# Kernel tuning notes

Hardware: AMD Instinct MI355X
Metric: run time of the kernel (lower is better)

## Reference

```python
import jax, jax.numpy as jnp
import numpy as np

B, E, CIN, O = 2, 50000, 8, 128


def _mesh_conv(x, gemm, w, b):
    # MeshCNN MeshConv: x (B,C,E), gemm (B,E,4) neighbor indices, w (O,C,5), b (O,)
    # gather 4 GeMM neighbors per edge, build 5 symmetric features, 1x5 conv
    neigh = jax.vmap(lambda xb, gb: xb[:, gb])(x, gemm)  # (B,C,E,4)
    f1, f2, f3, f4 = neigh[..., 0], neigh[..., 1], neigh[..., 2], neigh[..., 3]
    G = jnp.stack([x, f1 + f3, f2 + f4, jnp.abs(f1 - f3), jnp.abs(f2 - f4)], axis=-1)  # (B,C,E,5)
    return jnp.einsum('bces,ocs->boe', G, w) + b[None, :, None]


def _inorm(x, eps=1e-5):
    # InstanceNorm (no affine, biased variance) over the edge dim, per (batch, channel)
    m = jnp.mean(x, axis=-1, keepdims=True)
    v = jnp.var(x, axis=-1, keepdims=True)
    return (x - m) * jax.lax.rsqrt(v + eps)


def _conv1(x, w, b):
    # 1x1 Conv1d: x (B,C,E), w (O,C)
    return jnp.einsum('bce,oc->boe', x, w) + b[None, :, None]


def setup_inputs() -> dict:
    key = jax.random.key(0)
    ks = jax.random.split(key, 16)

    def W(k, shape, fan):
        return jax.random.normal(k, shape, jnp.float32) * np.float32(1.0 / np.sqrt(fan))

    d = {}
    d['fe'] = jax.random.normal(ks[0], (B, CIN, E), jnp.float32)
    d['gemm'] = jax.random.randint(ks[1], (B, E, 4), 0, E)
    # first-stage MeshConvs: geometry branch (5 ch) and position branch (3 ch)
    d['w_e1'] = W(ks[2], (O, 5, 5), 25);       d['b_e1'] = jnp.zeros((O,), jnp.float32)
    d['w_p1'] = W(ks[3], (O, 3, 5), 15);       d['b_p1'] = jnp.zeros((O,), jnp.float32)
    # residual-block MeshConvs (blocks=1)
    d['w_e2'] = W(ks[4], (O, O, 5), O * 5);    d['b_e2'] = jnp.zeros((O,), jnp.float32)
    d['w_p2'] = W(ks[5], (O, O, 5), O * 5);    d['b_p2'] = jnp.zeros((O,), jnp.float32)
    # Attn(in_dim=O)
    d['wa'] = W(ks[6], (O // 4, O), O);        d['ba'] = jnp.zeros((O // 4,), jnp.float32)
    d['wb'] = W(ks[7], (O // 4, O), O);        d['bb'] = jnp.zeros((O // 4,), jnp.float32)
    d['wal'] = W(ks[8], (O // 2, O // 2), O // 2);  d['bal'] = jnp.zeros((O // 2,), jnp.float32)
    d['wbl'] = W(ks[9], (O // 2, O // 2), O // 2);  d['bbl'] = jnp.zeros((O // 2,), jnp.float32)
    d['wat'] = W(ks[10], (O // 2, O // 2, 5), O // 2 * 5); d['bat'] = jnp.zeros((O // 2,), jnp.float32)
    d['wbt'] = W(ks[11], (O // 2, O // 2, 5), O // 2 * 5); d['bbt'] = jnp.zeros((O // 2,), jnp.float32)
    d['waf'] = W(ks[12], (O, O), O);           d['baf'] = jnp.zeros((O,), jnp.float32)
    d['wbf'] = W(ks[13], (O, O), O);           d['bbf'] = jnp.zeros((O,), jnp.float32)
    return d


def reference(fe, gemm, w_e1, b_e1, w_p1, b_p1, w_e2, b_e2, w_p2, b_p2,
              wa, ba, wb, bb, wal, bal, wbl, bbl, wat, bat, wbt, bbt,
              waf, baf, wbf, bbf):
    # DownConv (8-channel input path): split into edge (5) and point (3) branches
    fe_e, fe_p = fe[:, :5, :], fe[:, 5:, :]
    x1_e = jax.nn.relu(_inorm(_mesh_conv(fe_e, gemm, w_e1, b_e1)))
    x2_e = jax.nn.relu(_inorm(_mesh_conv(x1_e, gemm, w_e2, b_e2)) + x1_e)
    x1_p = jax.nn.relu(_inorm(_mesh_conv(fe_p, gemm, w_p1, b_p1)))
    x2_p = jax.nn.relu(_inorm(_mesh_conv(x1_p, gemm, w_p2, b_p2)) + x1_p)
    # Attn fusion
    x_all = jnp.concatenate([_conv1(x2_e, wa, ba), _conv1(x2_p, wb, bb)], axis=1)  # (B, O/2, E)
    x_a_two = jnp.concatenate([_conv1(x_all, wal, bal), _mesh_conv(x_all, gemm, wat, bat)], axis=1)
    x_b_two = jnp.concatenate([_conv1(x_all, wbl, bbl), _mesh_conv(x_all, gemm, wbt, bbt)], axis=1)
    wA = jax.nn.sigmoid(_inorm(_conv1(x_a_two, waf, baf)))  # (B,O,E)
    wB = jax.nn.sigmoid(_inorm(_conv1(x_b_two, wbf, bbf)))
    weights = jax.nn.softmax(jnp.stack([wA, wB], axis=1), axis=1)  # (B,2,O,E)
    agg = x2_e * weights[:, 0] + x2_p * weights[:, 1]
    # x2_ep = cat(x2_e, x2_p); also emit the attention-fused combine (before_pool)
    return jnp.concatenate([x2_e, x2_p, agg], axis=1)  # (B, 3*O, E)
```

## Files before the change

### kernel.cpp

```cpp
#include <hip/hip_runtime.h>
#include <cstdio>
#include <math.h>


#define E_TOT 50000
#define B_TOT 2
#define TILE_E 64
#define NBLK ((E_TOT + TILE_E - 1) / TILE_E)

typedef _Float16 half_t;
typedef __attribute__((ext_vector_type(4))) _Float16 h4;
typedef __attribute__((ext_vector_type(8))) _Float16 h8;
typedef __attribute__((ext_vector_type(4))) float f32x4;

__device__ __forceinline__ float sigmoidf_(float x) {
    return 1.0f / (1.0f + __expf(-x));
}
__device__ __forceinline__ h8 habs8(h8 x) {
    union { h8 h; unsigned int u[4]; } v;
    v.h = x;
#pragma unroll
    for (int i = 0; i < 4; ++i) v.u[i] &= 0x7FFF7FFFu;
    return v.h;
}

#define OFF_W1E   0
#define OFF_W1P   8192
#define OFF_WTE2  16384
#define OFF_WTP2  98304
#define OFF_WHA   180224
#define OFF_WHB   221184
#define OFF_WTA   262144
#define OFF_WTB   266240
#define OFF_WTAF  270336
#define OFF_WTBF  286720
#define WARENA_N  303104

__global__ __launch_bounds__(256)
void wprep_k(half_t* __restrict__ wa_,
             const float* __restrict__ w_e1, const float* __restrict__ w_p1,
             const float* __restrict__ w_e2, const float* __restrict__ w_p2,
             const float* __restrict__ wat,  const float* __restrict__ wbt,
             const float* __restrict__ wa,   const float* __restrict__ wb,
             const float* __restrict__ wal,  const float* __restrict__ wbl,
             const float* __restrict__ waf,  const float* __restrict__ wbf)
{
    int idx = blockIdx.x * 256 + threadIdx.x;
    switch (blockIdx.y) {
    case 0: if (idx < 8192) { int o = idx >> 6, k = idx & 63, s = k >> 3, cc = k & 7;
            float v = (s < 5 && cc < 5) ? w_e1[o * 25 + cc * 5 + s] : 0.f;
            wa_[OFF_W1E + idx] = (half_t)v; } break;
    case 1: if (idx < 8192) { int o = idx >> 6, k = idx & 63, s = k >> 3, cc = k & 7;
            float v = (s < 5 && cc >= 5) ? w_p1[o * 15 + (cc - 5) * 5 + s] : 0.f;
            wa_[OFF_W1P + idx] = (half_t)v; } break;
    case 2: if (idx < 81920) { int o = idx / 640, r = idx % 640, s = r >> 7, c = r & 127;
            wa_[OFF_WTE2 + idx] = (half_t)w_e2[(o * 128 + c) * 5 + s]; } break;
    case 3: if (idx < 81920) { int o = idx / 640, r = idx % 640, s = r >> 7, c = r & 127;
            wa_[OFF_WTP2 + idx] = (half_t)w_p2[(o * 128 + c) * 5 + s]; } break;
    case 4: if (idx < 40960) { int o = idx / 320, r = idx % 320, s = r >> 6, c = r & 63;
            float v = (o < 64) ? (s == 0 ? wal[o * 64 + c] : 0.f)
                               : wat[((o - 64) * 64 + c) * 5 + s];
            wa_[OFF_WHA + idx] = (half_t)v; } break;
    case 5: if (idx < 40960) { int o = idx / 320, r = idx % 320, s = r >> 6, c = r & 63;
            float v = (o < 64) ? (s == 0 ? wbl[o * 64 + c] : 0.f)
                               : wbt[((o - 64) * 64 + c) * 5 + s];
            wa_[OFF_WHB + idx] = (half_t)v; } break;
    case 6: if (idx < 4096)  wa_[OFF_WTA  + idx] = (half_t)wa[idx];  break;
    case 7: if (idx < 4096)  wa_[OFF_WTB  + idx] = (half_t)wb[idx];  break;
    case 8: if (idx < 16384) wa_[OFF_WTAF + idx] = (half_t)waf[idx]; break;
    case 9: if (idx < 16384) wa_[OFF_WTBF + idx] = (half_t)wbf[idx]; break;
    }
}

__global__ __launch_bounds__(256)
void transpose_in_k(const float* __restrict__ fe, float* __restrict__ fet)
{
    int b = blockIdx.z;
    int e = blockIdx.x * 256 + threadIdx.x;
    if (e >= E_TOT) return;
    float v[8];
#pragma unroll
    for (int c = 0; c < 8; ++c)
        v[c] = fe[((long)b * 8 + c) * E_TOT + e];
    float4* dst = (float4*)&fet[((long)b * E_TOT + e) * 8];
    dst[0] = make_float4(v[0], v[1], v[2], v[3]);
    dst[1] = make_float4(v[4], v[5], v[6], v[7]);
}

__global__ __launch_bounds__(512)
void mesh1_both_k(const float* __restrict__ fet, const int* __restrict__ gemm,
                  const half_t* __restrict__ war,
                  const float* __restrict__ be1, const float* __restrict__ bp1,
                  half_t* __restrict__ tmpe, half_t* __restrict__ tmpp,
                  float* __restrict__ parte, float* __restrict__ partp)
{
    __shared__ h8 Gl[64 * 8];
    __shared__ int nidx[64][4];

    const int tid  = threadIdx.x;
    const int b    = blockIdx.y;
    const int e0   = blockIdx.x * TILE_E;
    const int lane = tid & 63;
    const int wv   = tid >> 6;
    const int l15  = lane & 15;
    const int kg   = lane >> 4;
    const int br   = wv >> 2;
    const int o0   = (wv & 3) * 32;

    const float* xb = fet + (long)b * E_TOT * 8;

    if (tid < 256) {
        int e = tid >> 2, s = tid & 3;
        int eg = e0 + e;
        nidx[e][s] = (eg < E_TOT) ? gemm[((long)b * E_TOT + eg) * 4 + s] : 0;
    }
    __syncthreads();

    {
        int e = tid >> 3, g = tid & 7;
        int eg = e0 + e;
        int se = (eg < E_TOT) ? eg : 0;
        h8 r;
        if (g == 0) {
            const float* p = xb + (long)se * 8;
            float4 v0 = *(const float4*)p, v1 = *(const float4*)(p + 4);
            r[0] = (half_t)v0.x; r[1] = (half_t)v0.y; r[2] = (half_t)v0.z; r[3] = (half_t)v0.w;
            r[4] = (half_t)v1.x; r[5] = (half_t)v1.y; r[6] = (half_t)v1.z; r[7] = (half_t)v1.w;
        } else if (g <= 4) {
            int ia = (g == 1 || g == 3) ? 0 : 1;
            const float* pa = xb + (long)nidx[e][ia] * 8;
            const float* pb = xb + (long)nidx[e][ia + 2] * 8;
            float4 a0 = *(const float4*)pa, a1 = *(const float4*)(pa + 4);
            float4 b0 = *(const float4*)pb, b1 = *(const float4*)(pb + 4);
            float aa[8] = {a0.x, a0.y, a0.z, a0.w, a1.x, a1.y, a1.z, a1.w};
            float bb[8] = {b0.x, b0.y, b0.z, b0.w, b1.x, b1.y, b1.z, b1.w};
            if (g <= 2) {
#pragma unroll
                for (int j = 0; j < 8; ++j) r[j] = (half_t)(aa[j] + bb[j]);
            } else {
#pragma unroll
                for (int j = 0; j < 8; ++j) r[j] = (half_t)fabsf(aa[j] - bb[j]);
            }
        } else {
#pragma unroll
            for (int j = 0; j < 8; ++j) r[j] = (half_t)0.f;
        }
        Gl[(e * 8 + g) ^ (e & 7)] = r;
    }
    __syncthreads();

    f32x4 acc[4][2];
#pragma unroll
    for (int mt = 0; mt < 4; ++mt)
#pragma unroll
        for (int nt = 0; nt < 2; ++nt)
#pragma unroll
            for (int j = 0; j < 4; ++j) acc[mt][nt][j] = 0.f;

    const half_t* wt = war + (br ? OFF_W1P : OFF_W1E);
#pragma unroll
    for (int ks = 0; ks < 2; ++ks) {
        h8 bw[2];
#pragma unroll
        for (int nt = 0; nt < 2; ++nt)
            bw[nt] = *(const h8*)(wt + (long)(o0 + nt * 16 + l15) * 64 + ks * 32 + kg * 8);
#pragma unroll
        for (int mt = 0; mt < 4; ++mt) {
            int row = mt * 16 + l15;
            h8 a = Gl[row * 8 + ((ks * 4 + kg) ^ (row & 7))];
#pragma unroll
            for (int nt = 0; nt < 2; ++nt)
                acc[mt][nt] = __builtin_amdgcn_mfma_f32_16x16x32_f16(a, bw[nt], acc[mt][nt], 0, 0, 0);
        }
    }

    const float* bias = br ? bp1 : be1;
    half_t* yb = (br ? tmpp : tmpe) + (long)b * E_TOT * 128;
    float* part = br ? partp : parte;
    float bv[2], s1[2], s2[2];
#pragma unroll
    for (int nt = 0; nt < 2; ++nt) {
        bv[nt] = bias[o0 + nt * 16 + l15];
        s1[nt] = 0.f; s2[nt] = 0.f;
    }
#pragma unroll
    for (int mt = 0; mt < 4; ++mt) {
        int ebase = e0 + mt * 16 + (kg << 2);
#pragma unroll
        for (int j = 0; j < 4; ++j) {
            if (ebase + j < E_TOT) {
#pragma unroll
                for (int nt = 0; nt < 2; ++nt) {
                    float v = acc[mt][nt][j] + bv[nt];
                    yb[(long)(ebase + j) * 128 + o0 + nt * 16 + l15] = (half_t)v;
                    s1[nt] += v; s2[nt] += v * v;
                }
            }
        }
    }
#pragma unroll
    for (int nt = 0; nt < 2; ++nt) {
        s1[nt] += __shfl_xor(s1[nt], 16); s1[nt] += __shfl_xor(s1[nt], 32);
        s2[nt] += __shfl_xor(s2[nt], 16); s2[nt] += __shfl_xor(s2[nt], 32);
    }
    if (lane < 16) {
        long pb = ((long)b * NBLK + blockIdx.x) * 128;
#pragma unroll
        for (int nt = 0; nt < 2; ++nt) {
            part[(pb + o0 + nt * 16 + lane) * 2 + 0] = s1[nt];
            part[(pb + o0 + nt * 16 + lane) * 2 + 1] = s2[nt];
        }
    }
}

__global__ __launch_bounds__(512)
void mesh2_both_k(const half_t* __restrict__ x1e, const half_t* __restrict__ x1p,
                  const int* __restrict__ gemm, const half_t* __restrict__ war,
                  const float* __restrict__ be, const float* __restrict__ bp,
                  half_t* __restrict__ tmpe, half_t* __restrict__ tmpp,
                  float* __restrict__ parte, float* __restrict__ partp)
{
    __shared__ h8 GlA[64 * 16];
    __shared__ h8 GlB[64 * 16];
    __shared__ int nidx[64][4];

    const int tid  = threadIdx.x;
    const int br   = blockIdx.y;
    const int b    = blockIdx.z;
    const int e0   = blockIdx.x * TILE_E;
    const int lane = tid & 63;
    const int wv   = tid >> 6;
    const int l15  = lane & 15;
    const int kg   = lane >> 4;
    const int o0   = wv * 16;

    const half_t* xb = (br ? x1p : x1e) + (long)b * E_TOT * 128;
    const half_t* wt = war + (br ? OFF_WTP2 : OFF_WTE2);

    if (tid < 256) {
        int e = tid >> 2, s = tid & 3;
        int eg = e0 + e;
        nidx[e][s] = (eg < E_TOT) ? gemm[((long)b * E_TOT + eg) * 4 + s] : 0;
    }

    auto stage_self = [&](h8* dst) {
#pragma unroll
        for (int t = 0; t < 2; ++t) {
            int q = t * 512 + tid;
            int e = q >> 4, c8 = q & 15;
            int eg = e0 + e;
            int se = (eg < E_TOT) ? eg : 0;
            dst[(e * 16 + c8) ^ (e & 7)] = *(const h8*)(xb + (long)se * 128 + c8 * 8);
        }
    };
    auto stage_pair = [&](h8* dstS, h8* dstD, int ia, int ib) {
#pragma unroll
        for (int t = 0; t < 2; ++t) {
            int q = t * 512 + tid;
            int e = q >> 4, c8 = q & 15;
            int na = nidx[e][ia], nb = nidx[e][ib];
            h8 a  = *(const h8*)(xb + (long)na * 128 + c8 * 8);
            h8 bq = *(const h8*)(xb + (long)nb * 128 + c8 * 8);
            int slot = (e * 16 + c8) ^ (e & 7);
            dstS[slot] = a + bq;
            dstD[slot] = habs8(a - bq);
        }
    };

    f32x4 acc[4];
#pragma unroll
    for (int mt = 0; mt < 4; ++mt)
#pragma unroll
        for (int j = 0; j < 4; ++j) acc[mt][j] = 0.f;

    auto compute_chunk = [&](const h8* buf, int s) {
#pragma unroll
        for (int ks = 0; ks < 4; ++ks) {
            h8 bw = *(const h8*)(wt + ((long)(o0 + l15) * 5 + s) * 128 + ks * 32 + kg * 8);
#pragma unroll
            for (int mt = 0; mt < 4; ++mt) {
                int row = mt * 16 + l15;
                h8 a = buf[row * 16 + ((ks * 4 + kg) ^ (row & 7))];
                acc[mt] = __builtin_amdgcn_mfma_f32_16x16x32_f16(a, bw, acc[mt], 0, 0, 0);
            }
        }
    };

    stage_self(GlA);
    __syncthreads();
    compute_chunk(GlA, 0);
    __syncthreads();
    stage_pair(GlA, GlB, 0, 2);
    __syncthreads();
    compute_chunk(GlA, 1);
    compute_chunk(GlB, 3);
    __syncthreads();
    stage_pair(GlA, GlB, 1, 3);
    __syncthreads();
    compute_chunk(GlA, 2);
    compute_chunk(GlB, 4);

    const float* bias = br ? bp : be;
    half_t* yb = (br ? tmpp : tmpe) + (long)b * E_TOT * 128;
    float* part = br ? partp : parte;
    float bv = bias[o0 + l15];
    float s1 = 0.f, s2 = 0.f;
#pragma unroll
    for (int mt = 0; mt < 4; ++mt) {
        int ebase = e0 + mt * 16 + (kg << 2);
#pragma unroll
        for (int j = 0; j < 4; ++j) {
            if (ebase + j < E_TOT) {
                float v = acc[mt][j] + bv;
                yb[(long)(ebase + j) * 128 + o0 + l15] = (half_t)v;
                s1 += v; s2 += v * v;
            }
        }
    }
    s1 += __shfl_xor(s1, 16); s1 += __shfl_xor(s1, 32);
    s2 += __shfl_xor(s2, 16); s2 += __shfl_xor(s2, 32);
    if (lane < 16) {
        long pb = ((long)b * NBLK + blockIdx.x) * 128;
        part[(pb + o0 + lane) * 2 + 0] = s1;
        part[(pb + o0 + lane) * 2 + 1] = s2;
    }
}

__global__ __launch_bounds__(512)
void heads_k(const half_t* __restrict__ xall, const int* __restrict__ gemm,
             const half_t* __restrict__ war,
             const float* __restrict__ bal, const float* __restrict__ bbl,
             const float* __restrict__ bat, const float* __restrict__ bbt,
             half_t* __restrict__ xa2, half_t* __restrict__ xb2)
{
    __shared__ h8 GlA[64 * 8];
    __shared__ h8 GlB[64 * 8];
    __shared__ int nidx[64][4];

    const int tid  = threadIdx.x;
    const int br   = blockIdx.y;
    const int b    = blockIdx.z;
    const int e0   = blockIdx.x * TILE_E;
    const int lane = tid & 63;
    const int wv   = tid >> 6;
    const int l15  = lane & 15;
    const int kg   = lane >> 4;
    const int o0   = wv * 16;

    const half_t* xb = xall + (long)b * E_TOT * 64;
    const half_t* wt = war + (br ? OFF_WHB : OFF_WHA);

    if (tid < 256) {
        int e = tid >> 2, s = tid & 3;
        int eg = e0 + e;
        nidx[e][s] = (eg < E_TOT) ? gemm[((long)b * E_TOT + eg) * 4 + s] : 0;
    }

    auto stage_self = [&](h8* dst) {
        int q = tid;
        int e = q >> 3, c8 = q & 7;
        int eg = e0 + e;
        int se = (eg < E_TOT) ? eg : 0;
        dst[(e * 8 + c8) ^ (e & 7)] = *(const h8*)(xb + (long)se * 64 + c8 * 8);
    };
    auto stage_pair = [&](h8* dstS, h8* dstD, int ia, int ib) {
        int q = tid;
        int e = q >> 3, c8 = q & 7;
        int na = nidx[e][ia], nb = nidx[e][ib];
        h8 a  = *(const h8*)(xb + (long)na * 64 + c8 * 8);
        h8 bq = *(const h8*)(xb + (long)nb * 64 + c8 * 8);
        int slot = (e * 8 + c8) ^ (e & 7);
        dstS[slot] = a + bq;
        dstD[slot] = habs8(a - bq);
    };

    f32x4 acc[4];
#pragma unroll
    for (int mt = 0; mt < 4; ++mt)
#pragma unroll
        for (int j = 0; j < 4; ++j) acc[mt][j] = 0.f;

    auto compute_chunk = [&](const h8* buf, int s) {
#pragma unroll
        for (int ks = 0; ks < 2; ++ks) {
            h8 bw = *(const h8*)(wt + ((long)(o0 + l15) * 5 + s) * 64 + ks * 32 + kg * 8);
#pragma unroll
            for (int mt = 0; mt < 4; ++mt) {
                int row = mt * 16 + l15;
                h8 a = buf[row * 8 + ((ks * 4 + kg) ^ (row & 7))];
                acc[mt] = __builtin_amdgcn_mfma_f32_16x16x32_f16(a, bw, acc[mt], 0, 0, 0);
            }
        }
    };

    stage_self(GlA);
    __syncthreads();
    compute_chunk(GlA, 0);
    __syncthreads();
    stage_pair(GlA, GlB, 0, 2);
    __syncthreads();
    compute_chunk(GlA, 1);
    compute_chunk(GlB, 3);
    __syncthreads();
    stage_pair(GlA, GlB, 1, 3);
    __syncthreads();
    compute_chunk(GlA, 2);
    compute_chunk(GlB, 4);

    int o = o0 + l15;
    float bv = (o < 64) ? (br ? bbl[o] : bal[o]) : (br ? bbt[o - 64] : bat[o - 64]);
    half_t* yb = (br ? xb2 : xa2) + (long)b * E_TOT * 128;
#pragma unroll
    for (int mt = 0; mt < 4; ++mt) {
        int ebase = e0 + mt * 16 + (kg << 2);
#pragma unroll
        for (int j = 0; j < 4; ++j) {
            if (ebase + j < E_TOT)
                yb[(long)(ebase + j) * 128 + o] = (half_t)(acc[mt][j] + bv);
        }
    }
}

__global__ __launch_bounds__(512)
void gates_k(const half_t* __restrict__ xa2, const half_t* __restrict__ xb2,
             const half_t* __restrict__ war,
             const float* __restrict__ baf, const float* __restrict__ bbf,
             half_t* __restrict__ tmpe, half_t* __restrict__ tmpp,
             float* __restrict__ parte, float* __restrict__ partp)
{
    __shared__ h8 Gl[64 * 16];

    const int tid  = threadIdx.x;
    const int br   = blockIdx.y;
    const int b    = blockIdx.z;
    const int e0   = blockIdx.x * TILE_E;
    const int lane = tid & 63;
    const int wv   = tid >> 6;
    const int l15  = lane & 15;
    const int kg   = lane >> 4;
    const int o0   = wv * 16;

    const half_t* xb = (br ? xb2 : xa2) + (long)b * E_TOT * 128;
    const half_t* wt = war + (br ? OFF_WTBF : OFF_WTAF);

#pragma unroll
    for (int t = 0; t < 2; ++t) {
        int q = t * 512 + tid;
        int e = q >> 4, c8 = q & 15;
        int eg = e0 + e;
        int se = (eg < E_TOT) ? eg : 0;
        Gl[(e * 16 + c8) ^ (e & 7)] = *(const h8*)(xb + (long)se * 128 + c8 * 8);
    }
    __syncthreads();

    f32x4 acc[4];
#pragma unroll
    for (int mt = 0; mt < 4; ++mt)
#pragma unroll
        for (int j = 0; j < 4; ++j) acc[mt][j] = 0.f;

#pragma unroll
    for (int ks = 0; ks < 4; ++ks) {
        h8 bw = *(const h8*)(wt + (long)(o0 + l15) * 128 + ks * 32 + kg * 8);
#pragma unroll
        for (int mt = 0; mt < 4; ++mt) {
            int row = mt * 16 + l15;
            h8 a = Gl[row * 16 + ((ks * 4 + kg) ^ (row & 7))];
            acc[mt] = __builtin_amdgcn_mfma_f32_16x16x32_f16(a, bw, acc[mt], 0, 0, 0);
        }
    }

    const float* bias = br ? bbf : baf;
    half_t* yb = (br ? tmpp : tmpe) + (long)b * E_TOT * 128;
    float* part = br ? partp : parte;
    float bv = bias[o0 + l15];
    float s1 = 0.f, s2 = 0.f;
#pragma unroll
    for (int mt = 0; mt < 4; ++mt) {
        int ebase = e0 + mt * 16 + (kg << 2);
#pragma unroll
        for (int j = 0; j < 4; ++j) {
            if (ebase + j < E_TOT) {
                float v = acc[mt][j] + bv;
                yb[(long)(ebase + j) * 128 + o0 + l15] = (half_t)v;
                s1 += v; s2 += v * v;
            }
        }
    }
    s1 += __shfl_xor(s1, 16); s1 += __shfl_xor(s1, 32);
    s2 += __shfl_xor(s2, 16); s2 += __shfl_xor(s2, 32);
    if (lane < 16) {
        long pb = ((long)b * NBLK + blockIdx.x) * 128;
        part[(pb + o0 + lane) * 2 + 0] = s1;
        part[(pb + o0 + lane) * 2 + 1] = s2;
    }
}

__global__ __launch_bounds__(256)
void xall_k(const half_t* __restrict__ x2e, const half_t* __restrict__ x2p,
            const half_t* __restrict__ war,
            const float* __restrict__ ba, const float* __restrict__ bb,
            half_t* __restrict__ xall)
{
    __shared__ h8 Gl[64 * 16];

    const int tid  = threadIdx.x;
    const int br   = blockIdx.y;
    const int b    = blockIdx.z;
    const int e0   = blockIdx.x * TILE_E;
    const int lane = tid & 63;
    const int wv   = tid >> 6;
    const int l15  = lane & 15;
    const int kg   = lane >> 4;
    const int eoff = wv * 16;

    const half_t* xb = (br ? x2p : x2e) + (long)b * E_TOT * 128;
    const half_t* wt = war + (br ? OFF_WTB : OFF_WTA);

#pragma unroll
    for (int t = 0; t < 4; ++t) {
        int q = t * 256 + tid;
        int e = q >> 4, c8 = q & 15;
        int eg = e0 + e;
        int se = (eg < E_TOT) ? eg : 0;
        Gl[(e * 16 + c8) ^ (e & 7)] = *(const h8*)(xb + (long)se * 128 + c8 * 8);
    }
    __syncthreads();

    f32x4 acc[2];
#pragma unroll
    for (int nt = 0; nt < 2; ++nt)
#pragma unroll
        for (int j = 0; j < 4; ++j) acc[nt][j] = 0.f;

#pragma unroll
    for (int ks = 0; ks < 4; ++ks) {
        h8 bw[2];
#pragma unroll
        for (int nt = 0; nt < 2; ++nt)
            bw[nt] = *(const h8*)(wt + (long)(nt * 16 + l15) * 128 + ks * 32 + kg * 8);
        int row = eoff + l15;
        h8 a = Gl[row * 16 + ((ks * 4 + kg) ^ (row & 7))];
#pragma unroll
        for (int nt = 0; nt < 2; ++nt)
            acc[nt] = __builtin_amdgcn_mfma_f32_16x16x32_f16(a, bw[nt], acc[nt], 0, 0, 0);
    }

    const float* bias = br ? bb : ba;
    half_t* yb = xall + (long)b * E_TOT * 64;
    int oOff = br * 32;
#pragma unroll
    for (int nt = 0; nt < 2; ++nt) {
        float bv = bias[nt * 16 + l15];
        int ebase = e0 + eoff + (kg << 2);
#pragma unroll
        for (int j = 0; j < 4; ++j) {
            if (ebase + j < E_TOT)
                yb[(long)(ebase + j) * 64 + oOff + nt * 16 + l15] = (half_t)(acc[nt][j] + bv);
        }
    }
}

__global__ __launch_bounds__(256)
void stats2_k(const float* __restrict__ parte, const float* __restrict__ partp,
              float* __restrict__ statse, float* __restrict__ statsp)
{
    int g = blockIdx.x;
    int br = g >> 8, rem = g & 255, b = rem >> 7, o = rem & 127;
    const float* part = br ? partp : parte;
    float* stats = br ? statsp : statse;
    int tid = threadIdx.x;
    float s1 = 0.f, s2 = 0.f;
    for (int k = tid; k < NBLK; k += 256) {
        long base = (((long)b * NBLK + k) * 128 + o) * 2;
        s1 += part[base];
        s2 += part[base + 1];
    }
#pragma unroll
    for (int d = 1; d < 64; d <<= 1) {
        s1 += __shfl_xor(s1, d);
        s2 += __shfl_xor(s2, d);
    }
    __shared__ float r1[4], r2[4];
    int wv = tid >> 6;
    if ((tid & 63) == 0) { r1[wv] = s1; r2[wv] = s2; }
    __syncthreads();
    if (tid == 0) {
        s1 = r1[0] + r1[1] + r1[2] + r1[3];
        s2 = r2[0] + r2[1] + r2[2] + r2[3];
        float mean = s1 / (float)E_TOT;
        float var  = s2 / (float)E_TOT - mean * mean;
        var = fmaxf(var, 0.f);
        stats[(b * 128 + o) * 2 + 0] = mean;
        stats[(b * 128 + o) * 2 + 1] = rsqrtf(var + 1e-5f);
    }
}

__global__ __launch_bounds__(256)
void norm_act2_k(const half_t* __restrict__ tmpe, const half_t* __restrict__ tmpp,
                 const float* __restrict__ statse, const float* __restrict__ statsp,
                 half_t* __restrict__ x1e, half_t* __restrict__ x1p)
{
    const long PER = (long)B_TOT * E_TOT * 16;
    long q = (long)blockIdx.x * 256 + threadIdx.x;
    if (q >= 2 * PER) return;
    int br = (q >= PER);
    q -= (long)br * PER;
    const half_t* src = br ? tmpp : tmpe;
    const float* stats = br ? statsp : statse;
    half_t* dst = br ? x1p : x1e;
    long idx = q * 8;
    int c = (int)(idx & 127);
    int b = (int)((idx >> 7) / E_TOT);
    h8 v = *(const h8*)&src[idx];
    h8 r;
#pragma unroll
    for (int j = 0; j < 8; ++j) {
        float2 st = *(const float2*)&stats[(b * 128 + c + j) * 2];
        float t = ((float)v[j] - st.x) * st.y;
        r[j] = (half_t)fmaxf(t, 0.f);
    }
    *(h8*)&dst[idx] = r;
}

__global__ __launch_bounds__(256)
void normres2_k(const half_t* __restrict__ tmpe, const half_t* __restrict__ tmpp,
                const half_t* __restrict__ x1e, const half_t* __restrict__ x1p,
                const float* __restrict__ statse, const float* __restrict__ statsp,
                float* __restrict__ outb,
                half_t* __restrict__ x2e, half_t* __restrict__ x2p)
{
    __shared__ float T[32 * 68];
    int br = blockIdx.y >> 2, cg = blockIdx.y & 3;
    int b = blockIdx.z;
    int e0 = blockIdx.x * 64;
    int tid = threadIdx.x;
    const half_t* xin = br ? tmpp : tmpe;
    const half_t* res = br ? x1p : x1e;
    const float* stats = br ? statsp : statse;
    half_t* x2b = br ? x2p : x2e;
    int sect = br * 128;
#pragma unroll
    for (int i = 0; i < 2; ++i) {
        int q = tid + i * 256;
        int e = q >> 3, cq = q & 7;
        int eg = e0 + e;
        int se = (eg < E_TOT) ? eg : (E_TOT - 1);
        int c = cg * 32 + cq * 4;
        long base = ((long)b * E_TOT + se) * 128 + c;
        h4 v4 = *(const h4*)&xin[base];
        h4 r4 = *(const h4*)&res[base];
        h4 o4;
#pragma unroll
        for (int j = 0; j < 4; ++j) {
            float2 st = *(const float2*)&stats[(b * 128 + c + j) * 2];
            float t = ((float)v4[j] - st.x) * st.y + (float)r4[j];
            t = fmaxf(t, 0.f);
            T[(cq * 4 + j) * 68 + e] = t;
            o4[j] = (half_t)t;
        }
        if (eg < E_TOT) *(h4*)&x2b[base] = o4;
    }
    __syncthreads();
#pragma unroll
    for (int i = 0; i < 2; ++i) {
        int q = tid + i * 256;
        int cl = q >> 4, eq = q & 15;
        int e4 = e0 + eq * 4;
        int cglob = sect + cg * 32 + cl;
        float4 v = *(const float4*)&T[cl * 68 + eq * 4];
        long obase = ((long)b * 384 + cglob) * E_TOT + e4;
        if (e4 + 3 < E_TOT) {
            *(float4*)&outb[obase] = v;
        } else {
            const float* vp = &v.x;
            for (int j = 0; j < 4; ++j)
                if (e4 + j < E_TOT) outb[obase + j] = vp[j];
        }
    }
}

__global__ __launch_bounds__(256)
void gate_agg2_k(const half_t* __restrict__ tA, const half_t* __restrict__ tB,
                 const float* __restrict__ statsA, const float* __restrict__ statsB,
                 const half_t* __restrict__ x2e, const half_t* __restrict__ x2p,
                 float* __restrict__ outb)
{
    __shared__ float T[32 * 68];
    int b = blockIdx.z, cg = blockIdx.y;
    int e0 = blockIdx.x * 64;
    int tid = threadIdx.x;
#pragma unroll
    for (int i = 0; i < 2; ++i) {
        int q = tid + i * 256;
        int e = q >> 3, cq = q & 7;
        int eg = e0 + e;
        int se = (eg < E_TOT) ? eg : (E_TOT - 1);
        int c = cg * 32 + cq * 4;
        long base = ((long)b * E_TOT + se) * 128 + c;
        h4 a4 = *(const h4*)&tA[base];
        h4 b4 = *(const h4*)&tB[base];
        h4 xe4 = *(const h4*)&x2e[base];
        h4 xp4 = *(const h4*)&x2p[base];
#pragma unroll
        for (int j = 0; j < 4; ++j) {
            float2 sa = *(const float2*)&statsA[(b * 128 + c + j) * 2];
            float2 sb = *(const float2*)&statsB[(b * 128 + c + j) * 2];
            float na = sigmoidf_(((float)a4[j] - sa.x) * sa.y);
            float nb = sigmoidf_(((float)b4[j] - sb.x) * sb.y);
            float s = sigmoidf_(na - nb);
            T[(cq * 4 + j) * 68 + e] = (float)xe4[j] * s + (float)xp4[j] * (1.f - s);
        }
    }
    __syncthreads();
#pragma unroll
    for (int i = 0; i < 2; ++i) {
        int q = tid + i * 256;
        int cl = q >> 4, eq = q & 15;
        int e4 = e0 + eq * 4;
        int cglob = cg * 32 + cl;
        float4 v = *(const float4*)&T[cl * 68 + eq * 4];
        long ab = ((long)b * 384 + 256 + cglob) * E_TOT + e4;
        if (e4 + 3 < E_TOT) {
            *(float4*)&outb[ab] = v;
        } else {
            const float* vp = &v.x;
            for (int j = 0; j < 4; ++j)
                if (e4 + j < E_TOT) outb[ab + j] = vp[j];
        }
    }
}

extern "C" void kernel_launch(void* const* d_in, const int* in_sizes, int n_in,
                              void* d_out, int out_size, void* d_ws, size_t ws_size,
                              hipStream_t stream)
{
    const float* fe   = (const float*)d_in[0];
    const int*   gemm = (const int*)  d_in[1];
    const float* w_e1 = (const float*)d_in[2];  const float* b_e1 = (const float*)d_in[3];
    const float* w_p1 = (const float*)d_in[4];  const float* b_p1 = (const float*)d_in[5];
    const float* w_e2 = (const float*)d_in[6];  const float* b_e2 = (const float*)d_in[7];
    const float* w_p2 = (const float*)d_in[8];  const float* b_p2 = (const float*)d_in[9];
    const float* wa   = (const float*)d_in[10]; const float* ba   = (const float*)d_in[11];
    const float* wb   = (const float*)d_in[12]; const float* bb   = (const float*)d_in[13];
    const float* wal  = (const float*)d_in[14]; const float* bal  = (const float*)d_in[15];
    const float* wbl  = (const float*)d_in[16]; const float* bbl  = (const float*)d_in[17];
    const float* wat  = (const float*)d_in[18]; const float* bat  = (const float*)d_in[19];
    const float* wbt  = (const float*)d_in[20]; const float* bbt  = (const float*)d_in[21];
    const float* waf  = (const float*)d_in[22]; const float* baf  = (const float*)d_in[23];
    const float* wbf  = (const float*)d_in[24]; const float* bbf  = (const float*)d_in[25];
    float* out = (float*)d_out;

    const long EB = (long)E_TOT;

    char* wp = (char*)d_ws;
    auto alloc = [&](size_t bytes) -> void* {
        void* r = (void*)wp;
        wp += (bytes + 255) & ~(size_t)255;
        return r;
    };
    float*  FET    = (float*)alloc((size_t)B_TOT * EB * 8 * 4);
    half_t* TMP_E  = (half_t*)alloc((size_t)B_TOT * EB * 128 * 2);
    half_t* TMP_P  = (half_t*)alloc((size_t)B_TOT * EB * 128 * 2);
    half_t* X1E    = (half_t*)alloc((size_t)B_TOT * EB * 128 * 2);
    half_t* X1P    = (half_t*)alloc((size_t)B_TOT * EB * 128 * 2);
    half_t* X2E    = (half_t*)alloc((size_t)B_TOT * EB * 128 * 2);
    half_t* X2P    = (half_t*)alloc((size_t)B_TOT * EB * 128 * 2);
    half_t* XALL   = (half_t*)alloc((size_t)B_TOT * EB * 64 * 2);
    float*  PART_E = (float*)alloc((size_t)B_TOT * NBLK * 128 * 2 * 4);
    float*  PART_P = (float*)alloc((size_t)B_TOT * NBLK * 128 * 2 * 4);
    float*  STATSE = (float*)alloc((size_t)B_TOT * 128 * 2 * 4);
    float*  STATSP = (float*)alloc((size_t)B_TOT * 128 * 2 * 4);
    half_t* WAR    = (half_t*)alloc((size_t)WARENA_N * 2);

    if ((size_t)(wp - (char*)d_ws) > ws_size) {
        fprintf(stderr, "kernel_launch: ws too small (%zu < %zu)\n",
                ws_size, (size_t)(wp - (char*)d_ws));
        return;
    }

    half_t* XA2 = X1E;
    half_t* XB2 = X1P;

    dim3 blk256(256), blk512(512);
    dim3 gE2(NBLK, 2, B_TOT);
    dim3 gE1(NBLK, B_TOT);
    dim3 gT((E_TOT + 255) / 256, 1, B_TOT);
    dim3 gN8(NBLK, 8, B_TOT);
    dim3 gN4(NBLK, 4, B_TOT);
    int gA2 = (int)((2 * (long)B_TOT * EB * 16 + 255) / 256);

    wprep_k<<<dim3(320, 10, 1), blk256, 0, stream>>>(WAR,
        w_e1, w_p1, w_e2, w_p2, wat, wbt, wa, wb, wal, wbl, waf, wbf);
    transpose_in_k<<<gT, blk256, 0, stream>>>(fe, FET);

    mesh1_both_k<<<gE1, blk512, 0, stream>>>(FET, gemm, WAR, b_e1, b_p1,
        TMP_E, TMP_P, PART_E, PART_P);
    stats2_k<<<512, blk256, 0, stream>>>(PART_E, PART_P, STATSE, STATSP);
    norm_act2_k<<<gA2, blk256, 0, stream>>>(TMP_E, TMP_P, STATSE, STATSP, X1E, X1P);

    mesh2_both_k<<<gE2, blk512, 0, stream>>>(X1E, X1P, gemm, WAR, b_e2, b_p2,
        TMP_E, TMP_P, PART_E, PART_P);
    stats2_k<<<512, blk256, 0, stream>>>(PART_E, PART_P, STATSE, STATSP);
    normres2_k<<<gN8, blk256, 0, stream>>>(TMP_E, TMP_P, X1E, X1P, STATSE, STATSP,
        out, X2E, X2P);

    xall_k<<<gE2, blk256, 0, stream>>>(X2E, X2P, WAR, ba, bb, XALL);

    heads_k<<<gE2, blk512, 0, stream>>>(XALL, gemm, WAR, bal, bbl, bat, bbt, XA2, XB2);

    gates_k<<<gE2, blk512, 0, stream>>>(XA2, XB2, WAR, baf, bbf,
        TMP_E, TMP_P, PART_E, PART_P);
    stats2_k<<<512, blk256, 0, stream>>>(PART_E, PART_P, STATSE, STATSP);
    gate_agg2_k<<<gN4, blk256, 0, stream>>>(TMP_E, TMP_P, STATSE, STATSP,
        X2E, X2P, out);
}
```

Baseline: 363.1 us.

## Interleave x1 branches per edge and merge both branches into one gather block

Stores the two first-stage activations interleaved per edge (256 channels per row), so one block gathers neighbor rows for both edge and point branches in a single 512-byte access. Both branches are computed in one block with each wave covering 32 outputs, and the next neighbor pair is prefetched into registers during the MFMA compute of the current chunk. The heads kernel is restructured the same way so one block shares the gathered xall tile across both heads instead of gathering it twice. This cuts redundant random gathers and index loads, at the cost of more registers and LDS per block, a launch-bounds occupancy hint, and a strided write in the normalize kernel.

```diff
diff --git a/kernel.cpp b/kernel.cpp
--- a/kernel.cpp
+++ b/kernel.cpp
@@ -213,210 +213,259 @@
     }
 }
 
-__global__ __launch_bounds__(512)
-void mesh2_both_k(const half_t* __restrict__ x1e, const half_t* __restrict__ x1p,
-                  const int* __restrict__ gemm, const half_t* __restrict__ war,
-                  const float* __restrict__ be, const float* __restrict__ bp,
-                  half_t* __restrict__ tmpe, half_t* __restrict__ tmpp,
-                  float* __restrict__ parte, float* __restrict__ partp)
-{
-    __shared__ h8 GlA[64 * 16];
-    __shared__ h8 GlB[64 * 16];
+__global__ __launch_bounds__(512, 4)
+void mesh2i_k(const half_t* __restrict__ x1i, const int* __restrict__ gemm,
+              const half_t* __restrict__ war,
+              const float* __restrict__ be, const float* __restrict__ bp,
+              half_t* __restrict__ tmpe, half_t* __restrict__ tmpp,
+              float* __restrict__ parte, float* __restrict__ partp)
+{
+    __shared__ h8 B0[1024], B1[1024], B2[1024], B3[1024];
     __shared__ int nidx[64][4];
 
     const int tid  = threadIdx.x;
-    const int br   = blockIdx.y;
-    const int b    = blockIdx.z;
+    const int b    = blockIdx.y;
     const int e0   = blockIdx.x * TILE_E;
     const int lane = tid & 63;
     const int wv   = tid >> 6;
+    const int br   = wv >> 2;
+    const int o0   = (wv & 3) * 32;
     const int l15  = lane & 15;
     const int kg   = lane >> 4;
-    const int o0   = wv * 16;
-
-    const half_t* xb = (br ? x1p : x1e) + (long)b * E_TOT * 128;
-    const half_t* wt = war + (br ? OFF_WTP2 : OFF_WTE2);
+
+    const half_t* xb = x1i + (long)b * E_TOT * 256;
 
     if (tid < 256) {
         int e = tid >> 2, s = tid & 3;
         int eg = e0 + e;
         nidx[e][s] = (eg < E_TOT) ? gemm[((long)b * E_TOT + eg) * 4 + s] : 0;
     }
-
-    auto stage_self = [&](h8* dst) {
-#pragma unroll
-        for (int t = 0; t < 2; ++t) {
-            int q = t * 512 + tid;
-            int e = q >> 4, c8 = q & 15;
-            int eg = e0 + e;
-            int se = (eg < E_TOT) ? eg : 0;
-            dst[(e * 16 + c8) ^ (e & 7)] = *(const h8*)(xb + (long)se * 128 + c8 * 8);
-        }
-    };
-    auto stage_pair = [&](h8* dstS, h8* dstD, int ia, int ib) {
-#pragma unroll
-        for (int t = 0; t < 2; ++t) {
-            int q = t * 512 + tid;
-            int e = q >> 4, c8 = q & 15;
-            int na = nidx[e][ia], nb = nidx[e][ib];
-            h8 a  = *(const h8*)(xb + (long)na * 128 + c8 * 8);
-            h8 bq = *(const h8*)(xb + (long)nb * 128 + c8 * 8);
-            int slot = (e * 16 + c8) ^ (e & 7);
-            dstS[slot] = a + bq;
-            dstD[slot] = habs8(a - bq);
-        }
-    };
-
-    f32x4 acc[4];
+    __syncthreads();
+
+    int te[4], tc[4], tslot[4];
+#pragma unroll
+    for (int t = 0; t < 4; ++t) {
+        int q = t * 512 + tid;
+        te[t] = q >> 5; tc[t] = q & 31;
+        tslot[t] = (te[t] * 16 + (tc[t] & 15)) ^ (te[t] & 7);
+    }
+
+#pragma unroll
+    for (int t = 0; t < 4; ++t) {
+        int eg = e0 + te[t];
+        int se = (eg < E_TOT) ? eg : 0;
+        h8 v = *(const h8*)(xb + (long)se * 256 + tc[t] * 8);
+        ((tc[t] >> 4) ? B1 : B0)[tslot[t]] = v;
+    }
+    h8 rA[4], rB[4];
+#pragma unroll
+    for (int t = 0; t < 4; ++t) {
+        int na = nidx[te[t]][0], nb = nidx[te[t]][2];
+        rA[t] = *(const h8*)(xb + (long)na * 256 + tc[t] * 8);
+        rB[t] = *(const h8*)(xb + (long)nb * 256 + tc[t] * 8);
+    }
+    __syncthreads();
+
+    f32x4 acc[4][2];
 #pragma unroll
     for (int mt = 0; mt < 4; ++mt)
 #pragma unroll
-        for (int j = 0; j < 4; ++j) acc[mt][j] = 0.f;
-
-    auto compute_chunk = [&](const h8* buf, int s) {
+        for (int nt = 0; nt < 2; ++nt)
+#pragma unroll
+            for (int j = 0; j < 4; ++j) acc[mt][nt][j] = 0.f;
+
+    const half_t* wt = war + (br ? OFF_WTP2 : OFF_WTE2);
+    auto chunk = [&](const h8* bufE, const h8* bufP, int s) {
+        const h8* buf = br ? bufP : bufE;
 #pragma unroll
         for (int ks = 0; ks < 4; ++ks) {
-            h8 bw = *(const h8*)(wt + ((long)(o0 + l15) * 5 + s) * 128 + ks * 32 + kg * 8);
+            h8 bw0 = *(const h8*)(wt + ((long)(o0 + l15) * 5 + s) * 128 + ks * 32 + kg * 8);
+            h8 bw1 = *(const h8*)(wt + ((long)(o0 + 16 + l15) * 5 + s) * 128 + ks * 32 + kg * 8);
 #pragma unroll
             for (int mt = 0; mt < 4; ++mt) {
                 int row = mt * 16 + l15;
                 h8 a = buf[row * 16 + ((ks * 4 + kg) ^ (row & 7))];
-                acc[mt] = __builtin_amdgcn_mfma_f32_16x16x32_f16(a, bw, acc[mt], 0, 0, 0);
+                acc[mt][0] = __builtin_amdgcn_mfma_f32_16x16x32_f16(a, bw0, acc[mt][0], 0, 0, 0);
+                acc[mt][1] = __builtin_amdgcn_mfma_f32_16x16x32_f16(a, bw1, acc[mt][1], 0, 0, 0);
             }
         }
     };
 
-    stage_self(GlA);
-    __syncthreads();
-    compute_chunk(GlA, 0);
-    __syncthreads();
-    stage_pair(GlA, GlB, 0, 2);
-    __syncthreads();
-    compute_chunk(GlA, 1);
-    compute_chunk(GlB, 3);
-    __syncthreads();
-    stage_pair(GlA, GlB, 1, 3);
-    __syncthreads();
-    compute_chunk(GlA, 2);
-    compute_chunk(GlB, 4);
+    chunk(B0, B1, 0);
+    __syncthreads();
+
+#pragma unroll
+    for (int t = 0; t < 4; ++t) {
+        h8 sv = rA[t] + rB[t];
+        h8 dv = habs8(rA[t] - rB[t]);
+        if (tc[t] >> 4) { B3[tslot[t]] = sv; B1[tslot[t]] = dv; }
+        else            { B2[tslot[t]] = sv; B0[tslot[t]] = dv; }
+    }
+#pragma unroll
+    for (int t = 0; t < 4; ++t) {
+        int na = nidx[te[t]][1], nb = nidx[te[t]][3];
+        rA[t] = *(const h8*)(xb + (long)na * 256 + tc[t] * 8);
+        rB[t] = *(const h8*)(xb + (long)nb * 256 + tc[t] * 8);
+    }
+    __syncthreads();
+
+    chunk(B2, B3, 1);
+    chunk(B0, B1, 3);
+    __syncthreads();
+
+#pragma unroll
+    for (int t = 0; t < 4; ++t) {
+        h8 sv = rA[t] + rB[t];
+        h8 dv = habs8(rA[t] - rB[t]);
+        if (tc[t] >> 4) { B3[tslot[t]] = sv; B1[tslot[t]] = dv; }
+        else            { B2[tslot[t]] = sv; B0[tslot[t]] = dv; }
+    }
+    __syncthreads();
+
+    chunk(B2, B3, 2);
+    chunk(B0, B1, 4);
 
     const float* bias = br ? bp : be;
     half_t* yb = (br ? tmpp : tmpe) + (long)b * E_TOT * 128;
     float* part = br ? partp : parte;
-    float bv = bias[o0 + l15];
-    float s1 = 0.f, s2 = 0.f;
+    float bv0 = bias[o0 + l15], bv1 = bias[o0 + 16 + l15];
+    float s1a = 0.f, s2a = 0.f, s1b = 0.f, s2b = 0.f;
 #pragma unroll
     for (int mt = 0; mt < 4; ++mt) {
         int ebase = e0 + mt * 16 + (kg << 2);
 #pragma unroll
         for (int j = 0; j < 4; ++j) {
             if (ebase + j < E_TOT) {
-                float v = acc[mt][j] + bv;
-                yb[(long)(ebase + j) * 128 + o0 + l15] = (half_t)v;
-                s1 += v; s2 += v * v;
+                float v0 = acc[mt][0][j] + bv0;
+                float v1 = acc[mt][1][j] + bv1;
+                yb[(long)(ebase + j) * 128 + o0 + l15]      = (half_t)v0;
+                yb[(long)(ebase + j) * 128 + o0 + 16 + l15] = (half_t)v1;
+                s1a += v0; s2a += v0 * v0;
+                s1b += v1; s2b += v1 * v1;
             }
         }
     }
-    s1 += __shfl_xor(s1, 16); s1 += __shfl_xor(s1, 32);
-    s2 += __shfl_xor(s2, 16); s2 += __shfl_xor(s2, 32);
+    s1a += __shfl_xor(s1a, 16); s1a += __shfl_xor(s1a, 32);
+    s2a += __shfl_xor(s2a, 16); s2a += __shfl_xor(s2a, 32);
+    s1b += __shfl_xor(s1b, 16); s1b += __shfl_xor(s1b, 32);
+    s2b += __shfl_xor(s2b, 16); s2b += __shfl_xor(s2b, 32);
     if (lane < 16) {
         long pb = ((long)b * NBLK + blockIdx.x) * 128;
-        part[(pb + o0 + lane) * 2 + 0] = s1;
-        part[(pb + o0 + lane) * 2 + 1] = s2;
-    }
-}
-
-__global__ __launch_bounds__(512)
-void heads_k(const half_t* __restrict__ xall, const int* __restrict__ gemm,
-             const half_t* __restrict__ war,
-             const float* __restrict__ bal, const float* __restrict__ bbl,
-             const float* __restrict__ bat, const float* __restrict__ bbt,
-             half_t* __restrict__ xa2, half_t* __restrict__ xb2)
-{
-    __shared__ h8 GlA[64 * 8];
-    __shared__ h8 GlB[64 * 8];
+        part[(pb + o0 + lane) * 2 + 0]      = s1a;
+        part[(pb + o0 + lane) * 2 + 1]      = s2a;
+        part[(pb + o0 + 16 + lane) * 2 + 0] = s1b;
+        part[(pb + o0 + 16 + lane) * 2 + 1] = s2b;
+    }
+}
+
+__global__ __launch_bounds__(512, 4)
+void heads2_k(const half_t* __restrict__ xall, const int* __restrict__ gemm,
+              const half_t* __restrict__ war,
+              const float* __restrict__ bal, const float* __restrict__ bbl,
+              const float* __restrict__ bat, const float* __restrict__ bbt,
+              half_t* __restrict__ xa2, half_t* __restrict__ xb2)
+{
+    __shared__ h8 C0[512], C1[512], C2[512];
     __shared__ int nidx[64][4];
 
     const int tid  = threadIdx.x;
-    const int br   = blockIdx.y;
-    const int b    = blockIdx.z;
+    const int b    = blockIdx.y;
     const int e0   = blockIdx.x * TILE_E;
     const int lane = tid & 63;
     const int wv   = tid >> 6;
+    const int hd   = wv >> 2;
+    const int o0   = (wv & 3) * 32;
     const int l15  = lane & 15;
     const int kg   = lane >> 4;
-    const int o0   = wv * 16;
 
     const half_t* xb = xall + (long)b * E_TOT * 64;
-    const half_t* wt = war + (br ? OFF_WHB : OFF_WHA);
 
     if (tid < 256) {
         int e = tid >> 2, s = tid & 3;
         int eg = e0 + e;
         nidx[e][s] = (eg < E_TOT) ? gemm[((long)b * E_TOT + eg) * 4 + s] : 0;
     }
-
-    auto stage_self = [&](h8* dst) {
-        int q = tid;
-        int e = q >> 3, c8 = q & 7;
-        int eg = e0 + e;
+    __syncthreads();
+
+    const int te = tid >> 3, tc = tid & 7;
+    const int tslot = (te * 8 + tc) ^ (te & 7);
+
+    {
+        int eg = e0 + te;
         int se = (eg < E_TOT) ? eg : 0;
-        dst[(e * 8 + c8) ^ (e & 7)] = *(const h8*)(xb + (long)se * 64 + c8 * 8);
-    };
-    auto stage_pair = [&](h8* dstS, h8* dstD, int ia, int ib) {
-        int q = tid;
-        int e = q >> 3, c8 = q & 7;
-        int na = nidx[e][ia], nb = nidx[e][ib];
-        h8 a  = *(const h8*)(xb + (long)na * 64 + c8 * 8);
-        h8 bq = *(const h8*)(xb + (long)nb * 64 + c8 * 8);
-        int slot = (e * 8 + c8) ^ (e & 7);
-        dstS[slot] = a + bq;
-        dstD[slot] = habs8(a - bq);
-    };
-
-    f32x4 acc[4];
+        C0[tslot] = *(const h8*)(xb + (long)se * 64 + tc * 8);
+    }
+    h8 rA, rB;
+    {
+        int na = nidx[te][0], nb = nidx[te][2];
+        rA = *(const h8*)(xb + (long)na * 64 + tc * 8);
+        rB = *(const h8*)(xb + (long)nb * 64 + tc * 8);
+    }
+    __syncthreads();
+
+    f32x4 acc[4][2];
 #pragma unroll
     for (int mt = 0; mt < 4; ++mt)
 #pragma unroll
-        for (int j = 0; j < 4; ++j) acc[mt][j] = 0.f;
-
-    auto compute_chunk = [&](const h8* buf, int s) {
+        for (int nt = 0; nt < 2; ++nt)
+#pragma unroll
+            for (int j = 0; j < 4; ++j) acc[mt][nt][j] = 0.f;
+
+    const half_t* wt = war + (hd ? OFF_WHB : OFF_WHA);
+    auto chunk = [&](const h8* buf, int s) {
 #pragma unroll
         for (int ks = 0; ks < 2; ++ks) {
-            h8 bw = *(const h8*)(wt + ((long)(o0 + l15) * 5 + s) * 64 + ks * 32 + kg * 8);
+            h8 bw0 = *(const h8*)(wt + ((long)(o0 + l15) * 5 + s) * 64 + ks * 32 + kg * 8);
+            h8 bw1 = *(const h8*)(wt + ((long)(o0 + 16 + l15) * 5 + s) * 64 + ks * 32 + kg * 8);
 #pragma unroll
             for (int mt = 0; mt < 4; ++mt) {
                 int row = mt * 16 + l15;
                 h8 a = buf[row * 8 + ((ks * 4 + kg) ^ (row & 7))];
-                acc[mt] = __builtin_amdgcn_mfma_f32_16x16x32_f16(a, bw, acc[mt], 0, 0, 0);
+                acc[mt][0] = __builtin_amdgcn_mfma_f32_16x16x32_f16(a, bw0, acc[mt][0], 0, 0, 0);
+                acc[mt][1] = __builtin_amdgcn_mfma_f32_16x16x32_f16(a, bw1, acc[mt][1], 0, 0, 0);
             }
         }
     };
 
-    stage_self(GlA);
-    __syncthreads();
-    compute_chunk(GlA, 0);
-    __syncthreads();
-    stage_pair(GlA, GlB, 0, 2);
-    __syncthreads();
-    compute_chunk(GlA, 1);
-    compute_chunk(GlB, 3);
-    __syncthreads();
-    stage_pair(GlA, GlB, 1, 3);
-    __syncthreads();
-    compute_chunk(GlA, 2);
-    compute_chunk(GlB, 4);
-
-    int o = o0 + l15;
-    float bv = (o < 64) ? (br ? bbl[o] : bal[o]) : (br ? bbt[o - 64] : bat[o - 64]);
-    half_t* yb = (br ? xb2 : xa2) + (long)b * E_TOT * 128;
+    chunk(C0, 0);
+    __syncthreads();
+    {
+        C1[tslot] = rA + rB;
+        C2[tslot] = habs8(rA - rB);
+        int na = nidx[te][1], nb = nidx[te][3];
+        rA = *(const h8*)(xb + (long)na * 64 + tc * 8);
+        rB = *(const h8*)(xb + (long)nb * 64 + tc * 8);
+    }
+    __syncthreads();
+    chunk(C1, 1);
+    chunk(C2, 3);
+    __syncthreads();
+    {
+        C1[tslot] = rA + rB;
+        C2[tslot] = habs8(rA - rB);
+    }
+    __syncthreads();
+    chunk(C1, 2);
+    chunk(C2, 4);
+
+    half_t* yb = (hd ? xb2 : xa2) + (long)b * E_TOT * 128;
+    float bv[2];
+#pragma unroll
+    for (int nt = 0; nt < 2; ++nt) {
+        int o = o0 + nt * 16 + l15;
+        bv[nt] = (o < 64) ? (hd ? bbl[o] : bal[o]) : (hd ? bbt[o - 64] : bat[o - 64]);
+    }
 #pragma unroll
     for (int mt = 0; mt < 4; ++mt) {
         int ebase = e0 + mt * 16 + (kg << 2);
 #pragma unroll
         for (int j = 0; j < 4; ++j) {
-            if (ebase + j < E_TOT)
-                yb[(long)(ebase + j) * 128 + o] = (half_t)(acc[mt][j] + bv);
+            if (ebase + j < E_TOT) {
+#pragma unroll
+                for (int nt = 0; nt < 2; ++nt)
+                    yb[(long)(ebase + j) * 128 + o0 + nt * 16 + l15] =
+                        (half_t)(acc[mt][nt][j] + bv[nt]);
+            }
         }
     }
 }
@@ -599,7 +648,7 @@
 __global__ __launch_bounds__(256)
 void norm_act2_k(const half_t* __restrict__ tmpe, const half_t* __restrict__ tmpp,
                  const float* __restrict__ statse, const float* __restrict__ statsp,
-                 half_t* __restrict__ x1e, half_t* __restrict__ x1p)
+                 half_t* __restrict__ x1i)
 {
     const long PER = (long)B_TOT * E_TOT * 16;
     long q = (long)blockIdx.x * 256 + threadIdx.x;
@@ -608,10 +657,11 @@
     q -= (long)br * PER;
     const half_t* src = br ? tmpp : tmpe;
     const float* stats = br ? statsp : statse;
-    half_t* dst = br ? x1p : x1e;
     long idx = q * 8;
     int c = (int)(idx & 127);
-    int b = (int)((idx >> 7) / E_TOT);
+    long be = idx >> 7;
+    int b = (int)(be / E_TOT);
+    int e = (int)(be % E_TOT);
     h8 v = *(const h8*)&src[idx];
     h8 r;
 #pragma unroll
@@ -620,12 +670,12 @@
         float t = ((float)v[j] - st.x) * st.y;
         r[j] = (half_t)fmaxf(t, 0.f);
     }
-    *(h8*)&dst[idx] = r;
+    *(h8*)&x1i[((long)b * E_TOT + e) * 256 + br * 128 + c] = r;
 }
 
 __global__ __launch_bounds__(256)
 void normres2_k(const half_t* __restrict__ tmpe, const half_t* __restrict__ tmpp,
-                const half_t* __restrict__ x1e, const half_t* __restrict__ x1p,
+                const half_t* __restrict__ x1i,
                 const float* __restrict__ statse, const float* __restrict__ statsp,
                 float* __restrict__ outb,
                 half_t* __restrict__ x2e, half_t* __restrict__ x2p)
@@ -636,7 +686,6 @@
     int e0 = blockIdx.x * 64;
     int tid = threadIdx.x;
     const half_t* xin = br ? tmpp : tmpe;
-    const half_t* res = br ? x1p : x1e;
     const float* stats = br ? statsp : statse;
     half_t* x2b = br ? x2p : x2e;
     int sect = br * 128;
@@ -649,7 +698,7 @@
         int c = cg * 32 + cq * 4;
         long base = ((long)b * E_TOT + se) * 128 + c;
         h4 v4 = *(const h4*)&xin[base];
-        h4 r4 = *(const h4*)&res[base];
+        h4 r4 = *(const h4*)&x1i[((long)b * E_TOT + se) * 256 + br * 128 + c];
         h4 o4;
 #pragma unroll
         for (int j = 0; j < 4; ++j) {
@@ -762,8 +811,7 @@
     float*  FET    = (float*)alloc((size_t)B_TOT * EB * 8 * 4);
     half_t* TMP_E  = (half_t*)alloc((size_t)B_TOT * EB * 128 * 2);
     half_t* TMP_P  = (half_t*)alloc((size_t)B_TOT * EB * 128 * 2);
-    half_t* X1E    = (half_t*)alloc((size_t)B_TOT * EB * 128 * 2);
-    half_t* X1P    = (half_t*)alloc((size_t)B_TOT * EB * 128 * 2);
+    half_t* X1I    = (half_t*)alloc((size_t)B_TOT * EB * 256 * 2);
     half_t* X2E    = (half_t*)alloc((size_t)B_TOT * EB * 128 * 2);
     half_t* X2P    = (half_t*)alloc((size_t)B_TOT * EB * 128 * 2);
     half_t* XALL   = (half_t*)alloc((size_t)B_TOT * EB * 64 * 2);
@@ -779,12 +827,12 @@
         return;
     }
 
-    half_t* XA2 = X1E;
-    half_t* XB2 = X1P;
+    half_t* XA2 = X1I;
+    half_t* XB2 = X1I + (size_t)B_TOT * EB * 128;
 
     dim3 blk256(256), blk512(512);
+    dim3 gI(NBLK, B_TOT);
     dim3 gE2(NBLK, 2, B_TOT);
-    dim3 gE1(NBLK, B_TOT);
     dim3 gT((E_TOT + 255) / 256, 1, B_TOT);
     dim3 gN8(NBLK, 8, B_TOT);
     dim3 gN4(NBLK, 4, B_TOT);
@@ -794,20 +842,20 @@
         w_e1, w_p1, w_e2, w_p2, wat, wbt, wa, wb, wal, wbl, waf, wbf);
     transpose_in_k<<<gT, blk256, 0, stream>>>(fe, FET);
 
-    mesh1_both_k<<<gE1, blk512, 0, stream>>>(FET, gemm, WAR, b_e1, b_p1,
+    mesh1_both_k<<<gI, blk512, 0, stream>>>(FET, gemm, WAR, b_e1, b_p1,
         TMP_E, TMP_P, PART_E, PART_P);
     stats2_k<<<512, blk256, 0, stream>>>(PART_E, PART_P, STATSE, STATSP);
-    norm_act2_k<<<gA2, blk256, 0, stream>>>(TMP_E, TMP_P, STATSE, STATSP, X1E, X1P);
-
-    mesh2_both_k<<<gE2, blk512, 0, stream>>>(X1E, X1P, gemm, WAR, b_e2, b_p2,
+    norm_act2_k<<<gA2, blk256, 0, stream>>>(TMP_E, TMP_P, STATSE, STATSP, X1I);
+
+    mesh2i_k<<<gI, blk512, 0, stream>>>(X1I, gemm, WAR, b_e2, b_p2,
         TMP_E, TMP_P, PART_E, PART_P);
     stats2_k<<<512, blk256, 0, stream>>>(PART_E, PART_P, STATSE, STATSP);
-    normres2_k<<<gN8, blk256, 0, stream>>>(TMP_E, TMP_P, X1E, X1P, STATSE, STATSP,
+    normres2_k<<<gN8, blk256, 0, stream>>>(TMP_E, TMP_P, X1I, STATSE, STATSP,
         out, X2E, X2P);
 
     xall_k<<<gE2, blk256, 0, stream>>>(X2E, X2P, WAR, ba, bb, XALL);
 
-    heads_k<<<gE2, blk512, 0, stream>>>(XALL, gemm, WAR, bal, bbl, bat, bbt, XA2, XB2);
+    heads2_k<<<gI, blk512, 0, stream>>>(XALL, gemm, WAR, bal, bbl, bat, bbt, XA2, XB2);
 
     gates_k<<<gE2, blk512, 0, stream>>>(XA2, XB2, WAR, baf, bbf,
         TMP_E, TMP_P, PART_E, PART_P);
```

Result: slower. 375.7 us (+3.5%).
